# Kernel optimization log

Measured on AMD Instinct MI355X. Metric: run time of the kernel, lower is better.

## Reference

```python
import jax, jax.numpy as jnp
import numpy as np

B, S, V, D, F, H, L = 2, 1024, 32000, 768, 3072, 12, 6
DH = D // H


def layer_norm(x, g, b, eps=1e-5):
    mu = jnp.mean(x, axis=-1, keepdims=True)
    var = jnp.mean((x - mu) ** 2, axis=-1, keepdims=True)
    return (x - mu) / jnp.sqrt(var + eps) * g + b


def setup_inputs() -> dict:
    key = jax.random.key(0)
    ks = jax.random.split(key, 20)
    s = 0.02  # init scale
    p = {
        'x': jax.random.randint(ks[0], (B, S), 0, V),
        'tok_emb': jax.random.normal(ks[1], (V, D), jnp.float32) * s,
        'pos_emb': jax.random.normal(ks[2], (S, D), jnp.float32) * s,
        'Wq': jax.random.normal(ks[3], (L, D, D), jnp.float32) * s,
        'bq': jnp.zeros((L, D), jnp.float32),
        'Wk': jax.random.normal(ks[4], (L, D, D), jnp.float32) * s,
        'bk': jnp.zeros((L, D), jnp.float32),
        'Wv': jax.random.normal(ks[5], (L, D, D), jnp.float32) * s,
        'bv': jnp.zeros((L, D), jnp.float32),
        'Wo': jax.random.normal(ks[6], (L, D, D), jnp.float32) * s,
        'bo': jnp.zeros((L, D), jnp.float32),
        'ln1_g': jnp.ones((L, D), jnp.float32),
        'ln1_b': jnp.zeros((L, D), jnp.float32),
        'W1': jax.random.normal(ks[7], (L, D, F), jnp.float32) * s,
        'b1': jnp.zeros((L, F), jnp.float32),
        'W2': jax.random.normal(ks[8], (L, F, D), jnp.float32) * s,
        'b2': jnp.zeros((L, D), jnp.float32),
        'ln2_g': jnp.ones((L, D), jnp.float32),
        'ln2_b': jnp.zeros((L, D), jnp.float32),
        'Wf': jax.random.normal(ks[9], (D, V), jnp.float32) * s,
        'bf': jnp.zeros((V,), jnp.float32),
    }
    return p


def reference(x, tok_emb, pos_emb, Wq, bq, Wk, bk, Wv, bv, Wo, bo,
              ln1_g, ln1_b, W1, b1, W2, b2, ln2_g, ln2_b, Wf, bf):
    hset = tok_emb[x] + pos_emb[None, :x.shape[1], :]  # [B,S,D]
    scale = 1.0 / jnp.sqrt(jnp.float32(D))  # note: original scales by sqrt(d_k)=sqrt(d_model)
    for i in range(L):
        q = (hset @ Wq[i] + bq[i]).reshape(B, S, H, DH).transpose(0, 2, 1, 3)
        k = (hset @ Wk[i] + bk[i]).reshape(B, S, H, DH).transpose(0, 2, 1, 3)
        v = (hset @ Wv[i] + bv[i]).reshape(B, S, H, DH).transpose(0, 2, 1, 3)
        scores = jnp.einsum('bhqd,bhkd->bhqk', q, k) * scale
        probs = jax.nn.softmax(scores, axis=-1)
        o = jnp.einsum('bhqk,bhkd->bhqd', probs, v)
        o = o.transpose(0, 2, 1, 3).reshape(B, S, D)
        attn = o @ Wo[i] + bo[i]
        h1 = layer_norm(attn + hset, ln1_g[i], ln1_b[i])
        ff = jax.nn.gelu(h1 @ W1[i] + b1[i], approximate=False) @ W2[i] + b2[i]
        hset = layer_norm(ff + h1, ln2_g[i], ln2_b[i])
    logits = hset @ Wf + bf
    log_probs = jax.nn.log_softmax(logits, axis=-1)
    return (log_probs, hset)
```

## Files before the change

kernel.cpp:

```cpp
#include <hip/hip_runtime.h>
#include <hip/hip_bf16.h>
#include <math.h>

#define B_ 2
#define S_ 1024
#define V_ 32000
#define D_ 768
#define F_ 3072
#define H_ 12
#define L_ 6
#define DH_ 64
#define BS_ (B_*S_)
#define NQKV_ 2304
#define KVB_ 128

typedef __attribute__((ext_vector_type(8))) short short8;
typedef __attribute__((ext_vector_type(4))) float f32x4;

__device__ __forceinline__ unsigned short f2b(float f) {
    union { __hip_bfloat16 h; unsigned short u; } cv;
    cv.h = __float2bfloat16(f);
    return cv.u;
}

__device__ __forceinline__ void store_bf4(__hip_bfloat16* p, float a, float b, float c, float d) {
    unsigned long long pk = (unsigned long long)f2b(a)
        | ((unsigned long long)f2b(b) << 16)
        | ((unsigned long long)f2b(c) << 32)
        | ((unsigned long long)f2b(d) << 48);
    *(unsigned long long*)p = pk;
}

__device__ __forceinline__ void gld16(const void* g, void* l) {
    __builtin_amdgcn_global_load_lds(
        (const __attribute__((address_space(1))) unsigned int*)g,
        (__attribute__((address_space(3))) unsigned int*)l,
        16, 0, 0);
}

__global__ void embed_k(const int* __restrict__ x, const float* __restrict__ tok,
                        const float* __restrict__ pos, float* __restrict__ h,
                        __hip_bfloat16* __restrict__ hbf) {
    int bs = blockIdx.x;
    int s = bs % S_;
    int t = x[bs];
    for (int d = threadIdx.x; d < D_; d += blockDim.x) {
        float v = tok[(size_t)t * D_ + d] + pos[(size_t)s * D_ + d];
        h[(size_t)bs * D_ + d] = v;
        hbf[(size_t)bs * D_ + d] = __float2bfloat16(v);
    }
}

__global__ __launch_bounds__(256) void transp_k(const float* __restrict__ src, size_t sl,
                                                __hip_bfloat16* __restrict__ dst, size_t dl,
                                                int N, int K) {
    const float* S = src + (size_t)blockIdx.z * sl;
    __hip_bfloat16* Dp = dst + (size_t)blockIdx.z * dl;
    __shared__ float T[32][33];
    const int k0 = blockIdx.y * 32, n0 = blockIdx.x * 32;
    const int tid = threadIdx.x;
    const int r = tid >> 3, c4 = (tid & 7) * 4;
    float4 vv = *(const float4*)&S[(size_t)(k0 + r) * N + n0 + c4];
    T[r][c4 + 0] = vv.x; T[r][c4 + 1] = vv.y; T[r][c4 + 2] = vv.z; T[r][c4 + 3] = vv.w;
    __syncthreads();
    store_bf4(&Dp[(size_t)(n0 + r) * K + k0 + c4],
              T[c4 + 0][r], T[c4 + 1][r], T[c4 + 2][r], T[c4 + 3][r]);
}

__global__ void bcat_k(const float* __restrict__ bq, const float* __restrict__ bk,
                       const float* __restrict__ bv, float* __restrict__ dst) {
    int l = blockIdx.x;
    for (int j = threadIdx.x; j < D_; j += blockDim.x) {
        dst[(size_t)l * NQKV_ + j]          = bq[(size_t)l * D_ + j];
        dst[(size_t)l * NQKV_ + D_ + j]     = bk[(size_t)l * D_ + j];
        dst[(size_t)l * NQKV_ + 2 * D_ + j] = bv[(size_t)l * D_ + j];
    }
}

template<int BM, int BN, int ACT, bool WF32, bool WBF, bool SW, bool XS, bool WVT>
__global__ __launch_bounds__(256) void mgemm_k(const __hip_bfloat16* __restrict__ A,
                                               const __hip_bfloat16* __restrict__ Bt,
                                               const float* __restrict__ bias,
                                               float* __restrict__ Cf,
                                               __hip_bfloat16* __restrict__ Cb,
                                               __hip_bfloat16* __restrict__ vTp,
                                               int M, int N, int K) {
    constexpr int WM = BM / 2, WN = BN / 2;
    constexpr int FM = WM / 16, FN = WN / 16;
    __shared__ __hip_bfloat16 Al[BM * 64];
    __shared__ __hip_bfloat16 Bl[BN * 64];
    const int tid = threadIdx.x;
    const int wid = tid >> 6, lane = tid & 63;
    const int wr = wid >> 1, wc = wid & 1;
    const int lrow = lane & 15, kq = lane >> 4;

    int bx = blockIdx.x, by = blockIdx.y;
    if (XS) {
        const int gx = gridDim.x;
        const int nwg = gx * gridDim.y;
        const int lin = by * gx + bx;
        const int logical = (lin & 7) * (nwg >> 3) + (lin >> 3);
        bx = logical % gx;
        by = logical / gx;
    }
    const int row0 = (SW ? bx : by) * BM;
    const int col0 = (SW ? by : bx) * BN;

    f32x4 acc[FM][FN];
    #pragma unroll
    for (int i = 0; i < FM; ++i)
        #pragma unroll
        for (int j = 0; j < FN; ++j)
            acc[i][j] = (f32x4){0.f, 0.f, 0.f, 0.f};

    const int srow = (lane >> 3);
    const int scol = ((lane & 7) ^ srow) * 8;

    for (int kk = 0; kk < K; kk += 64) {
        #pragma unroll
        for (int i = 0; i < BM / 32; ++i)
            gld16(A + (size_t)(row0 + i * 32 + wid * 8 + srow) * K + kk + scol,
                  &Al[(i * 32 + wid * 8) * 64]);
        #pragma unroll
        for (int i = 0; i < BN / 32; ++i)
            gld16(Bt + (size_t)(col0 + i * 32 + wid * 8 + srow) * K + kk + scol,
                  &Bl[(i * 32 + wid * 8) * 64]);
        __syncthreads();

        #pragma unroll
        for (int kc = 0; kc < 2; ++kc) {
            short8 af[FM], bfr[FN];
            #pragma unroll
            for (int i = 0; i < FM; ++i) {
                const int row = wr * WM + i * 16 + lrow;
                af[i] = *(const short8*)((const char*)Al + row * 128
                          + ((kc * 64 + kq * 16) ^ ((row & 7) << 4)));
            }
            #pragma unroll
            for (int j = 0; j < FN; ++j) {
                const int row = wc * WN + j * 16 + lrow;
                bfr[j] = *(const short8*)((const char*)Bl + row * 128
                          + ((kc * 64 + kq * 16) ^ ((row & 7) << 4)));
            }
            #pragma unroll
            for (int i = 0; i < FM; ++i)
                #pragma unroll
                for (int j = 0; j < FN; ++j)
                    acc[i][j] = __builtin_amdgcn_mfma_f32_16x16x32_bf16(af[i], bfr[j], acc[i][j], 0, 0, 0);
        }
        __syncthreads();
    }

    #pragma unroll
    for (int i = 0; i < FM; ++i)
        #pragma unroll
        for (int j = 0; j < FN; ++j) {
            const int col = col0 + wc * WN + j * 16 + lrow;
            const float bv = bias[col];
            const int rowq = row0 + wr * WM + i * 16 + kq * 4;
            if (WVT && col >= 1536) {
                const int cv = col - 1536;
                const int bh = (rowq >> 10) * H_ + (cv >> 6);
                store_bf4(&vTp[((size_t)bh * DH_ + (cv & 63)) * S_ + (rowq & 1023)],
                          acc[i][j][0] + bv, acc[i][j][1] + bv,
                          acc[i][j][2] + bv, acc[i][j][3] + bv);
            } else {
                #pragma unroll
                for (int r = 0; r < 4; ++r) {
                    const int row = rowq + r;
                    float vv = acc[i][j][r] + bv;
                    if (ACT == 1) vv = 0.5f * vv * (1.0f + erff(vv * 0.70710678118654752f));
                    if (WVT && col < D_) vv *= 0.03608439182435161f;
                    if (WF32) Cf[(size_t)row * N + col] = vv;
                    if (WBF)  Cb[(size_t)row * N + col] = __float2bfloat16(vv);
                }
            }
        }
}

__global__ __launch_bounds__(256) void gemm_k(const float* __restrict__ A,
                                              const float* __restrict__ W,
                                              const float* __restrict__ bias,
                                              float* __restrict__ Cout,
                                              int M, int N, int K) {
    __shared__ float As[64][16];
    __shared__ float Bs[16][64];
    const int tid = threadIdx.x;
    const int tx = tid & 15, ty = tid >> 4;
    const int row0 = blockIdx.y * 64, col0 = blockIdx.x * 64;
    float acc[4][4] = {};

    for (int kk = 0; kk < K; kk += 16) {
        #pragma unroll
        for (int it = 0; it < 4; ++it) {
            int idx = tid + it * 256;
            int m = idx >> 4, k = idx & 15;
            As[m][k] = A[(size_t)(row0 + m) * K + kk + k];
            int r = idx >> 6, c = idx & 63;
            Bs[r][c] = W[(size_t)(kk + r) * N + col0 + c];
        }
        __syncthreads();
        #pragma unroll
        for (int k = 0; k < 16; ++k) {
            float a[4], b[4];
            #pragma unroll
            for (int i = 0; i < 4; ++i) a[i] = As[ty * 4 + i][k];
            #pragma unroll
            for (int j = 0; j < 4; ++j) b[j] = Bs[k][tx * 4 + j];
            #pragma unroll
            for (int i = 0; i < 4; ++i)
                #pragma unroll
                for (int j = 0; j < 4; ++j)
                    acc[i][j] += a[i] * b[j];
        }
        __syncthreads();
    }

    #pragma unroll
    for (int i = 0; i < 4; ++i) {
        int r = row0 + ty * 4 + i;
        #pragma unroll
        for (int j = 0; j < 4; ++j) {
            int c = col0 + tx * 4 + j;
            Cout[(size_t)r * N + c] = acc[i][j] + bias[c];
        }
    }
}

__global__ __launch_bounds__(256) void fattn_k(const __hip_bfloat16* __restrict__ qkv,
                                               const __hip_bfloat16* __restrict__ vT,
                                               __hip_bfloat16* __restrict__ o) {
    const int qt0 = blockIdx.x * 64;
    const int bh = blockIdx.y;
    const int b = bh / H_, hh = bh % H_;
    const size_t rb = (size_t)b * S_;
    const int hoff = hh * DH_;

    __shared__ __hip_bfloat16 Ks[2][KVB_ * 64];
    __shared__ __hip_bfloat16 Vt[2][64 * KVB_];
    __shared__ __hip_bfloat16 Ps[64 * KVB_];

    const int tid = threadIdx.x;
    const int w = tid >> 6, lane = tid & 63;
    const int lr = lane & 15, lk = lane >> 4;
    const size_t vbase = (size_t)bh * DH_ * S_;

    short8 aq[2];
    {
        const int qrow = qt0 + w * 16 + lr;
        #pragma unroll
        for (int kc = 0; kc < 2; ++kc)
            aq[kc] = *(const short8*)&qkv[(rb + qrow) * NQKV_ + hoff + kc * 32 + lk * 8];
    }

    f32x4 oacc[4];
    float m_i[4], l_i[4];
    #pragma unroll
    for (int r = 0; r < 4; ++r) {
        oacc[r] = (f32x4){0.f, 0.f, 0.f, 0.f};
        m_i[r] = -1e30f;
        l_i[r] = 0.f;
    }

    auto stage = [&](int bi, int kt0) {
        #pragma unroll
        for (int t = 0; t < 4; ++t) {
            const int r0 = w * 32 + t * 8;
            const int r = r0 + (lane >> 3);
            const int cs = (lane & 7) ^ ((r & 7) ^ ((r >> 3) & 7));
            gld16(&qkv[(rb + kt0 + r) * NQKV_ + D_ + hoff + cs * 8], &Ks[bi][r0 * 64]);
        }
        #pragma unroll
        for (int t = 0; t < 4; ++t) {
            const int d0 = w * 16 + t * 4;
            const int d = d0 + (lane >> 4);
            const int cs = (lane & 15) ^ (d & 15);
            gld16(&vT[vbase + (size_t)d * S_ + kt0 + cs * 8], &Vt[bi][d0 * 128]);
        }
    };

    stage(0, 0);
    int cur = 0;
    for (int kt0 = 0; kt0 < S_; kt0 += KVB_) {
        __syncthreads();
        if (kt0 + KVB_ < S_) stage(cur ^ 1, kt0 + KVB_);
        const char* Kb = (const char*)Ks[cur];
        const char* Vb = (const char*)Vt[cur];

        f32x4 s[8];
        #pragma unroll
        for (int j = 0; j < 8; ++j) s[j] = (f32x4){0.f, 0.f, 0.f, 0.f};
        __builtin_amdgcn_s_setprio(1);
        #pragma unroll
        for (int kc = 0; kc < 2; ++kc) {
            #pragma unroll
            for (int j = 0; j < 8; ++j) {
                int kr = j * 16 + lr;
                short8 bk = *(const short8*)(Kb + kr * 128
                              + ((kc * 64 + lk * 16) ^ ((((kr & 7) ^ ((kr >> 3) & 7)) << 4))));
                s[j] = __builtin_amdgcn_mfma_f32_16x16x32_bf16(aq[kc], bk, s[j], 0, 0, 0);
            }
        }
        __builtin_amdgcn_s_setprio(0);

        float tmax[4];
        #pragma unroll
        for (int r = 0; r < 4; ++r) {
            float t = s[0][r];
            #pragma unroll
            for (int j = 1; j < 8; ++j) t = fmaxf(t, s[j][r]);
            tmax[r] = t;
        }
        float excess = fmaxf(fmaxf(tmax[0] - m_i[0], tmax[1] - m_i[1]),
                             fmaxf(tmax[2] - m_i[2], tmax[3] - m_i[3]));
        if (!__all(excess <= 8.0f)) {
            #pragma unroll
            for (int r = 0; r < 4; ++r) {
                float tm = tmax[r];
                #pragma unroll
                for (int off = 1; off <= 8; off <<= 1)
                    tm = fmaxf(tm, __shfl_xor(tm, off));
                float mnew = fmaxf(m_i[r], tm);
                float corr = __expf(m_i[r] - mnew);
                m_i[r] = mnew;
                l_i[r] *= corr;
                #pragma unroll
                for (int jd = 0; jd < 4; ++jd) oacc[jd][r] *= corr;
            }
        }
        #pragma unroll
        for (int r = 0; r < 4; ++r) {
            float psum = 0.f;
            const int prow = w * 16 + lk * 4 + r;
            #pragma unroll
            for (int j = 0; j < 8; ++j) {
                float p = __expf(s[j][r] - m_i[r]);
                psum += p;
                *(__hip_bfloat16*)((char*)Ps + prow * 256
                    + (((j * 16 + lr) * 2) ^ ((prow & 15) << 4))) = __float2bfloat16(p);
            }
            #pragma unroll
            for (int off = 1; off <= 8; off <<= 1)
                psum += __shfl_xor(psum, off);
            l_i[r] += psum;
        }

        __builtin_amdgcn_s_setprio(1);
        #pragma unroll
        for (int ks = 0; ks < 4; ++ks) {
            const int prow = w * 16 + lr;
            short8 pa = *(const short8*)((const char*)Ps + prow * 256
                          + ((ks * 64 + lk * 16) ^ ((prow & 15) << 4)));
            #pragma unroll
            for (int jd = 0; jd < 4; ++jd) {
                int vr = jd * 16 + lr;
                short8 vb = *(const short8*)(Vb + vr * 256
                              + ((ks * 64 + lk * 16) ^ ((vr & 15) << 4)));
                oacc[jd] = __builtin_amdgcn_mfma_f32_16x16x32_bf16(pa, vb, oacc[jd], 0, 0, 0);
            }
        }
        __builtin_amdgcn_s_setprio(0);
        cur ^= 1;
    }

    #pragma unroll
    for (int r = 0; r < 4; ++r) {
        float inv = 1.0f / l_i[r];
        const int row = qt0 + w * 16 + lk * 4 + r;
        #pragma unroll
        for (int jd = 0; jd < 4; ++jd)
            o[(rb + row) * (size_t)D_ + hoff + jd * 16 + lr] = __float2bfloat16(oacc[jd][r] * inv);
    }
}

__global__ __launch_bounds__(256) void addln_k(const float* __restrict__ a,
                                               const float* __restrict__ b,
                                               const float* __restrict__ g,
                                               const float* __restrict__ beta,
                                               float* __restrict__ out,
                                               __hip_bfloat16* __restrict__ out_bf) {
    const int r = blockIdx.x;
    const int tid = threadIdx.x;
    const int wid = tid >> 6, lane = tid & 63;
    __shared__ float w1[4], w2[4];
    float xv[3];
    float s1 = 0.f, s2 = 0.f;
    #pragma unroll
    for (int i = 0; i < 3; ++i) {
        int d = tid + i * 256;
        xv[i] = a[(size_t)r * D_ + d] + b[(size_t)r * D_ + d];
        s1 += xv[i];
        s2 += xv[i] * xv[i];
    }
    #pragma unroll
    for (int off = 1; off <= 32; off <<= 1) {
        s1 += __shfl_xor(s1, off);
        s2 += __shfl_xor(s2, off);
    }
    if (lane == 0) { w1[wid] = s1; w2[wid] = s2; }
    __syncthreads();
    s1 = w1[0] + w1[1] + w1[2] + w1[3];
    s2 = w2[0] + w2[1] + w2[2] + w2[3];
    float mu = s1 * (1.0f / D_);
    float var = s2 * (1.0f / D_) - mu * mu;
    float rstd = rsqrtf(var + 1e-5f);
    #pragma unroll
    for (int i = 0; i < 3; ++i) {
        int d = tid + i * 256;
        float v = (xv[i] - mu) * rstd * g[d] + beta[d];
        out[(size_t)r * D_ + d] = v;
        out_bf[(size_t)r * D_ + d] = __float2bfloat16(v);
    }
}

__global__ __launch_bounds__(256) void lsm_k(float* __restrict__ lp) {
    const int r = blockIdx.x;
    const int tid = threadIdx.x;
    const int wid = tid >> 6, lane = tid & 63;
    __shared__ float wm[4], wl[4];
    float* row = lp + (size_t)r * V_;
    float mt = -1e30f, lt = 0.f;
    for (int i = tid * 4; i < V_; i += 1024) {
        float4 v = *(const float4*)&row[i];
        float c = fmaxf(fmaxf(v.x, v.y), fmaxf(v.z, v.w));
        if (c > mt) { lt *= __expf(mt - c); mt = c; }
        lt += __expf(v.x - mt) + __expf(v.y - mt) + __expf(v.z - mt) + __expf(v.w - mt);
    }
    #pragma unroll
    for (int off = 1; off <= 32; off <<= 1) {
        float m2 = __shfl_xor(mt, off), l2 = __shfl_xor(lt, off);
        float M = fmaxf(mt, m2);
        lt = lt * __expf(mt - M) + l2 * __expf(m2 - M);
        mt = M;
    }
    if (lane == 0) { wm[wid] = mt; wl[wid] = lt; }
    __syncthreads();
    float M4 = fmaxf(fmaxf(wm[0], wm[1]), fmaxf(wm[2], wm[3]));
    float L4 = wl[0] * __expf(wm[0] - M4) + wl[1] * __expf(wm[1] - M4)
             + wl[2] * __expf(wm[2] - M4) + wl[3] * __expf(wm[3] - M4);
    float sub = M4 + __logf(L4);
    for (int i = tid * 4; i < V_; i += 1024) {
        float4 v = *(const float4*)&row[i];
        v.x -= sub; v.y -= sub; v.z -= sub; v.w -= sub;
        *(float4*)&row[i] = v;
    }
}

extern "C" void kernel_launch(void* const* d_in, const int* in_sizes, int n_in,
                              void* d_out, int out_size, void* d_ws, size_t ws_size,
                              hipStream_t stream) {
    const int*   x    = (const int*)  d_in[0];
    const float* tok  = (const float*)d_in[1];
    const float* pos  = (const float*)d_in[2];
    const float* Wq   = (const float*)d_in[3];
    const float* bq   = (const float*)d_in[4];
    const float* Wk   = (const float*)d_in[5];
    const float* bk   = (const float*)d_in[6];
    const float* Wv   = (const float*)d_in[7];
    const float* bv   = (const float*)d_in[8];
    const float* Wo   = (const float*)d_in[9];
    const float* bo   = (const float*)d_in[10];
    const float* ln1g = (const float*)d_in[11];
    const float* ln1b = (const float*)d_in[12];
    const float* W1   = (const float*)d_in[13];
    const float* b1   = (const float*)d_in[14];
    const float* W2   = (const float*)d_in[15];
    const float* b2   = (const float*)d_in[16];
    const float* ln2g = (const float*)d_in[17];
    const float* ln2b = (const float*)d_in[18];
    const float* Wf   = (const float*)d_in[19];
    const float* bff  = (const float*)d_in[20];

    float* out = (float*)d_out;
    const size_t HS = (size_t)BS_ * D_;

    __hip_bfloat16* qkv_bf = (__hip_bfloat16*)out;
    __hip_bfloat16* vT     = (__hip_bfloat16*)(out + 2359296);
    __hip_bfloat16* att_bf = (__hip_bfloat16*)(out + 4718592);
    float* tmp   = out + 5505024;
    float* h1    = out + 7077888;
    __hip_bfloat16* h1_bf  = (__hip_bfloat16*)(out + 8650752);
    __hip_bfloat16* ff_bf  = (__hip_bfloat16*)(out + 9437184);
    __hip_bfloat16* h_bf   = (__hip_bfloat16*)(out + 12582912);
    __hip_bfloat16* Wqkv_t = (__hip_bfloat16*)(out + 13369344);
    __hip_bfloat16* Wo_t   = (__hip_bfloat16*)(out + 18677760);
    __hip_bfloat16* W1_t   = (__hip_bfloat16*)(out + 20447232);
    __hip_bfloat16* W2_t   = (__hip_bfloat16*)(out + 27525120);
    float* bqkv  = out + 34603008;
    float* h     = out + (size_t)BS_ * V_;

    const bool ws_ok = ws_size >= 52297728ULL;
    __hip_bfloat16* Wf_t   = (__hip_bfloat16*)d_ws;
    __hip_bfloat16* hbf_ws = (__hip_bfloat16*)((char*)d_ws + 49152000);

    const size_t DD = (size_t)D_ * D_, DF = (size_t)D_ * F_;
    const size_t QKVL = (size_t)NQKV_ * D_;
    transp_k<<<dim3(D_/32, D_/32, L_), 256, 0, stream>>>(Wq, DD, Wqkv_t,          QKVL, D_, D_);
    transp_k<<<dim3(D_/32, D_/32, L_), 256, 0, stream>>>(Wk, DD, Wqkv_t + DD,     QKVL, D_, D_);
    transp_k<<<dim3(D_/32, D_/32, L_), 256, 0, stream>>>(Wv, DD, Wqkv_t + 2 * DD, QKVL, D_, D_);
    transp_k<<<dim3(D_/32, D_/32, L_), 256, 0, stream>>>(Wo, DD, Wo_t,            DD,   D_, D_);
    transp_k<<<dim3(F_/32, D_/32, L_), 256, 0, stream>>>(W1, DF, W1_t,            DF,   F_, D_);
    transp_k<<<dim3(D_/32, F_/32, L_), 256, 0, stream>>>(W2, DF, W2_t,            DF,   D_, F_);
    bcat_k<<<L_, 256, 0, stream>>>(bq, bk, bv, bqkv);
    if (ws_ok)
        transp_k<<<dim3(V_/32, D_/32, 1), 256, 0, stream>>>(Wf, 0, Wf_t, 0, V_, D_);

    embed_k<<<BS_, 256, 0, stream>>>(x, tok, pos, h, h_bf);

    const dim3 gQKV(NQKV_/128, BS_/64);
    const dim3 gFF1(F_/128,    BS_/64);
    const dim3 gOUT64(D_/64,   BS_/64);
    const dim3 gA(S_/64, B_*H_);
    for (int i = 0; i < L_; ++i) {
        mgemm_k<64,128,0,false,true,false,false,true><<<gQKV, 256, 0, stream>>>(
            h_bf, Wqkv_t + (size_t)i * QKVL, bqkv + (size_t)i * NQKV_, nullptr, qkv_bf, vT, BS_, NQKV_, D_);
        fattn_k<<<gA, 256, 0, stream>>>(qkv_bf, vT, att_bf);
        mgemm_k<64,64,0,true,false,false,false,false><<<gOUT64, 256, 0, stream>>>(
            att_bf, Wo_t + (size_t)i * DD, bo + (size_t)i * D_, tmp, nullptr, nullptr, BS_, D_, D_);
        addln_k<<<BS_, 256, 0, stream>>>(tmp, h, ln1g + (size_t)i * D_, ln1b + (size_t)i * D_, h1, h1_bf);
        mgemm_k<64,128,1,false,true,false,false,false><<<gFF1, 256, 0, stream>>>(
            h1_bf, W1_t + (size_t)i * DF, b1 + (size_t)i * F_, nullptr, ff_bf, nullptr, BS_, F_, D_);
        mgemm_k<64,64,0,true,false,false,false,false><<<gOUT64, 256, 0, stream>>>(
            ff_bf, W2_t + (size_t)i * DF, b2 + (size_t)i * D_, tmp, nullptr, nullptr, BS_, D_, F_);
        __hip_bfloat16* obf = (i == L_ - 1 && ws_ok) ? hbf_ws : h_bf;
        addln_k<<<BS_, 256, 0, stream>>>(tmp, h1, ln2g + (size_t)i * D_, ln2b + (size_t)i * D_, h, obf);
    }

    if (ws_ok) {
        mgemm_k<128,128,0,true,false,true,true,false><<<dim3(BS_/128, V_/128), 256, 0, stream>>>(
            hbf_ws, Wf_t, bff, out, nullptr, nullptr, BS_, V_, D_);
    } else {
        gemm_k<<<dim3(V_/64, BS_/64), 256, 0, stream>>>(h, Wf, bff, out, BS_, V_, D_);
    }
    lsm_k<<<BS_, 256, 0, stream>>>(out);
}
```

Measured before the change: 1.163 ms.

## Write vocab logits as bf16 in place and expand in log-softmax

The final vocab projection now stores its logits as bf16 into the first half of each fp32 output row, using a row stride of 2*V bf16 elements. A new log-softmax kernel reads the bf16 row, computes an online max and sum, then expands to fp32 in place. It walks the chunks in reverse with a barrier so that bf16 data is read before the fp32 writes overwrite it. This halves the GEMM's output write traffic and the log-softmax read traffic. The cost is that logits are rounded to bf16 before log_softmax, which lowers output precision.

```diff
diff --git a/kernel.cpp b/kernel.cpp
--- a/kernel.cpp
+++ b/kernel.cpp
@@ -23,6 +23,12 @@
     return cv.u;
 }
 
+__device__ __forceinline__ float b2f(unsigned short u) {
+    union { unsigned int i; float f; } cv;
+    cv.i = ((unsigned int)u) << 16;
+    return cv.f;
+}
+
 __device__ __forceinline__ void store_bf4(__hip_bfloat16* p, float a, float b, float c, float d) {
     unsigned long long pk = (unsigned long long)f2b(a)
         | ((unsigned long long)f2b(b) << 16)
@@ -84,7 +90,7 @@
                                                float* __restrict__ Cf,
                                                __hip_bfloat16* __restrict__ Cb,
                                                __hip_bfloat16* __restrict__ vTp,
-                                               int M, int N, int K) {
+                                               int M, int N, int K, int ldcb) {
     constexpr int WM = BM / 2, WN = BN / 2;
     constexpr int FM = WM / 16, FN = WN / 16;
     __shared__ __hip_bfloat16 Al[BM * 64];
@@ -172,7 +178,7 @@
                     if (ACT == 1) vv = 0.5f * vv * (1.0f + erff(vv * 0.70710678118654752f));
                     if (WVT && col < D_) vv *= 0.03608439182435161f;
                     if (WF32) Cf[(size_t)row * N + col] = vv;
-                    if (WBF)  Cb[(size_t)row * N + col] = __float2bfloat16(vv);
+                    if (WBF)  Cb[(size_t)row * ldcb + col] = __float2bfloat16(vv);
                 }
             }
         }
@@ -443,6 +449,60 @@
         float4 v = *(const float4*)&row[i];
         v.x -= sub; v.y -= sub; v.z -= sub; v.w -= sub;
         *(float4*)&row[i] = v;
+    }
+}
+
+__global__ __launch_bounds__(256) void lsmx_k(float* __restrict__ lp) {
+    const int r = blockIdx.x;
+    const int tid = threadIdx.x;
+    const int wid = tid >> 6, lane = tid & 63;
+    __shared__ float wm[4], wl[4];
+    float* row = lp + (size_t)r * V_;
+    const __hip_bfloat16* brow = (const __hip_bfloat16*)row;
+
+    float mt = -1e30f, lt = 0.f;
+    for (int i = tid * 8; i < V_; i += 2048) {
+        short8 v = *(const short8*)&brow[i];
+        #pragma unroll
+        for (int j = 0; j < 8; ++j) {
+            float f = b2f((unsigned short)v[j]);
+            if (f > mt) { lt *= __expf(mt - f); mt = f; }
+            lt += __expf(f - mt);
+        }
+    }
+    #pragma unroll
+    for (int off = 1; off <= 32; off <<= 1) {
+        float m2 = __shfl_xor(mt, off), l2 = __shfl_xor(lt, off);
+        float M = fmaxf(mt, m2);
+        lt = lt * __expf(mt - M) + l2 * __expf(m2 - M);
+        mt = M;
+    }
+    if (lane == 0) { wm[wid] = mt; wl[wid] = lt; }
+    __syncthreads();
+    float M4 = fmaxf(fmaxf(wm[0], wm[1]), fmaxf(wm[2], wm[3]));
+    float L4 = wl[0] * __expf(wm[0] - M4) + wl[1] * __expf(wm[1] - M4)
+             + wl[2] * __expf(wm[2] - M4) + wl[3] * __expf(wm[3] - M4);
+    float sub = M4 + __logf(L4);
+
+    for (int ci = 15; ci >= 0; --ci) {
+        const int c = ci * 2048 + tid * 8;
+        const bool act = (c < V_);
+        short8 v;
+        if (act) v = *(const short8*)&brow[c];
+        __syncthreads();
+        if (act) {
+            float4 o0, o1;
+            o0.x = b2f((unsigned short)v[0]) - sub;
+            o0.y = b2f((unsigned short)v[1]) - sub;
+            o0.z = b2f((unsigned short)v[2]) - sub;
+            o0.w = b2f((unsigned short)v[3]) - sub;
+            o1.x = b2f((unsigned short)v[4]) - sub;
+            o1.y = b2f((unsigned short)v[5]) - sub;
+            o1.z = b2f((unsigned short)v[6]) - sub;
+            o1.w = b2f((unsigned short)v[7]) - sub;
+            *(float4*)&row[c] = o0;
+            *(float4*)&row[c + 4] = o1;
+        }
     }
 }
 
@@ -513,24 +573,25 @@
     const dim3 gA(S_/64, B_*H_);
     for (int i = 0; i < L_; ++i) {
         mgemm_k<64,128,0,false,true,false,false,true><<<gQKV, 256, 0, stream>>>(
-            h_bf, Wqkv_t + (size_t)i * QKVL, bqkv + (size_t)i * NQKV_, nullptr, qkv_bf, vT, BS_, NQKV_, D_);
+            h_bf, Wqkv_t + (size_t)i * QKVL, bqkv + (size_t)i * NQKV_, nullptr, qkv_bf, vT, BS_, NQKV_, D_, NQKV_);
         fattn_k<<<gA, 256, 0, stream>>>(qkv_bf, vT, att_bf);
         mgemm_k<64,64,0,true,false,false,false,false><<<gOUT64, 256, 0, stream>>>(
-            att_bf, Wo_t + (size_t)i * DD, bo + (size_t)i * D_, tmp, nullptr, nullptr, BS_, D_, D_);
+            att_bf, Wo_t + (size_t)i * DD, bo + (size_t)i * D_, tmp, nullptr, nullptr, BS_, D_, D_, D_);
         addln_k<<<BS_, 256, 0, stream>>>(tmp, h, ln1g + (size_t)i * D_, ln1b + (size_t)i * D_, h1, h1_bf);
         mgemm_k<64,128,1,false,true,false,false,false><<<gFF1, 256, 0, stream>>>(
-            h1_bf, W1_t + (size_t)i * DF, b1 + (size_t)i * F_, nullptr, ff_bf, nullptr, BS_, F_, D_);
+            h1_bf, W1_t + (size_t)i * DF, b1 + (size_t)i * F_, nullptr, ff_bf, nullptr, BS_, F_, D_, F_);
         mgemm_k<64,64,0,true,false,false,false,false><<<gOUT64, 256, 0, stream>>>(
-            ff_bf, W2_t + (size_t)i * DF, b2 + (size_t)i * D_, tmp, nullptr, nullptr, BS_, D_, F_);
+            ff_bf, W2_t + (size_t)i * DF, b2 + (size_t)i * D_, tmp, nullptr, nullptr, BS_, D_, F_, D_);
         __hip_bfloat16* obf = (i == L_ - 1 && ws_ok) ? hbf_ws : h_bf;
         addln_k<<<BS_, 256, 0, stream>>>(tmp, h1, ln2g + (size_t)i * D_, ln2b + (size_t)i * D_, h, obf);
     }
 
     if (ws_ok) {
-        mgemm_k<128,128,0,true,false,true,true,false><<<dim3(BS_/128, V_/128), 256, 0, stream>>>(
-            hbf_ws, Wf_t, bff, out, nullptr, nullptr, BS_, V_, D_);
+        mgemm_k<128,128,0,false,true,true,true,false><<<dim3(BS_/128, V_/128), 256, 0, stream>>>(
+            hbf_ws, Wf_t, bff, nullptr, (__hip_bfloat16*)out, nullptr, BS_, V_, D_, 2 * V_);
+        lsmx_k<<<BS_, 256, 0, stream>>>(out);
     } else {
         gemm_k<<<dim3(V_/64, BS_/64), 256, 0, stream>>>(h, Wf, bff, out, BS_, V_, D_);
-    }
-    lsm_k<<<BS_, 256, 0, stream>>>(out);
-}
+        lsm_k<<<BS_, 256, 0, stream>>>(out);
+    }
+}
```

After: 1.107 ms. -4.8%, faster.
